# Optimization experiments

Hardware: AMD Instinct MI355X
Metric: run time of the kernel (lower is better)

## Reference

```python
import jax, jax.numpy as jnp
import numpy as np

N, IN, OUT = 262144, 256, 256
EPS_MIN = 1e-10


def setup_inputs() -> dict:
    key = jax.random.key(0)
    k1, k2, k3 = jax.random.split(key, 3)
    x = jax.random.normal(k1, (N, IN), dtype=jnp.float32)
    weight = jax.random.normal(k2, (OUT, IN), dtype=jnp.float32) * 0.05
    bias = jax.random.normal(k3, (OUT,), dtype=jnp.float32) * 0.02
    return {"x": x, "weight": weight, "bias": bias}


def reference(x, weight, bias):
    # Mean-center weight rows and input rows (dim=1 in torch)
    wc = weight - jnp.mean(weight, axis=1, keepdims=True)          # [out, in]
    xc = x - jnp.mean(x, axis=1, keepdims=True)                    # [N, in]
    # temp_linear with all-ones weight == row-sum of xc^2, broadcast over out
    x_len = jax.lax.stop_gradient(
        jnp.sqrt(jnp.sum(xc * xc, axis=1, keepdims=True)))          # [N, 1]
    # temp_linear(ones_like(x)) with weight wc^2 == row-sum of wc^2 per out
    w_len = jax.lax.stop_gradient(
        jnp.sqrt(jnp.sum(wc * wc, axis=1)))                          # [out]
    # Correlation: centered GEMM, normalized, clamped; bias added after clamp
    corr = jnp.einsum('ni,oi->no', xc, wc) / (x_len * w_len[None, :])
    out = jnp.clip(corr, EPS_MIN, None) + bias[None, :]
    return out
```

## Files before the change

kernel.cpp:

```cpp
#include <hip/hip_runtime.h>
#include <hip/hip_bf16.h>


#define K_DIM 256
#define N_OUT 256
#define BM 64
#define LDS_STRIDE 264

typedef __attribute__((ext_vector_type(8))) __bf16 bf16x8;
typedef __attribute__((ext_vector_type(8))) unsigned short u16x8;
typedef __attribute__((ext_vector_type(4))) float f32x4;

__device__ __forceinline__ unsigned short f2bf(float f) {
    union { float f; unsigned u; } v; v.f = f;
    unsigned r = v.u + 0x7FFFu + ((v.u >> 16) & 1u);
    return (unsigned short)(r >> 16);
}

__global__ __launch_bounds__(64) void prep_w(const float* __restrict__ w,
                                             unsigned short* __restrict__ wcb) {
    int o = blockIdx.x;
    int lane = threadIdx.x;
    f32x4 v = *((const f32x4*)(w + (size_t)o * K_DIM) + lane);
    float s  = v.x + v.y + v.z + v.w;
    float s2 = v.x*v.x + v.y*v.y + v.z*v.z + v.w*v.w;
#pragma unroll
    for (int off = 32; off >= 1; off >>= 1) {
        s  += __shfl_xor(s,  off);
        s2 += __shfl_xor(s2, off);
    }
    float mean  = s * (1.0f / 256.0f);
    float var   = s2 - s * mean;
    float scale = rsqrtf(fmaxf(var, 1e-30f));
    ushort4 b;
    b.x = f2bf((v.x - mean) * scale);
    b.y = f2bf((v.y - mean) * scale);
    b.z = f2bf((v.z - mean) * scale);
    b.w = f2bf((v.w - mean) * scale);
    *(ushort4*)(wcb + (size_t)o * K_DIM + lane * 4) = b;
}

__global__ __launch_bounds__(256, 4) void pcc_gemm(const float* __restrict__ x,
                                                   const unsigned short* __restrict__ wcb,
                                                   const float* __restrict__ bias,
                                                   float* __restrict__ out) {
    __shared__ unsigned short xs[BM * LDS_STRIDE];
    __shared__ float nrm[BM];

    const int t    = threadIdx.x;
    const int wave = t >> 6;
    const int lane = t & 63;
    const int l15  = lane & 15;
    const int q    = lane >> 4;
    const size_t row0 = (size_t)blockIdx.x * BM;

    const int srow = wave * 16 + l15;
    const float* rp = x + (row0 + srow) * K_DIM + q * 64;

    f32x4 v[16];
#pragma unroll
    for (int j = 0; j < 16; ++j) v[j] = ((const f32x4*)rp)[j];

    const int n0 = wave * 64;
    float bv[4];
#pragma unroll
    for (int ni = 0; ni < 4; ++ni) bv[ni] = bias[n0 + ni * 16 + l15];

    unsigned short* wp = xs + srow * LDS_STRIDE + q * 64;
#pragma unroll
    for (int j = 0; j < 8; ++j) {
        u16x8 p;
        p[0] = f2bf(v[2*j].x);   p[1] = f2bf(v[2*j].y);
        p[2] = f2bf(v[2*j].z);   p[3] = f2bf(v[2*j].w);
        p[4] = f2bf(v[2*j+1].x); p[5] = f2bf(v[2*j+1].y);
        p[6] = f2bf(v[2*j+1].z); p[7] = f2bf(v[2*j+1].w);
        *(u16x8*)(wp + j * 8) = p;
    }

    float s = 0.f, s2 = 0.f;
#pragma unroll
    for (int j = 0; j < 16; ++j) {
        s += v[j].x + v[j].y + v[j].z + v[j].w;
        s2 = fmaf(v[j].x, v[j].x, s2);
        s2 = fmaf(v[j].y, v[j].y, s2);
        s2 = fmaf(v[j].z, v[j].z, s2);
        s2 = fmaf(v[j].w, v[j].w, s2);
    }
    s  += __shfl_xor(s, 16);  s  += __shfl_xor(s, 32);
    s2 += __shfl_xor(s2, 16); s2 += __shfl_xor(s2, 32);
    float var = s2 - s * s * (1.0f / 256.0f);
    float inv = rsqrtf(fmaxf(var, 1e-30f));
    if (q == 0) nrm[srow] = inv;
    __syncthreads();

    f32x4 acc[4][4];
#pragma unroll
    for (int mi = 0; mi < 4; ++mi)
#pragma unroll
        for (int ni = 0; ni < 4; ++ni)
            acc[mi][ni] = (f32x4){0.f, 0.f, 0.f, 0.f};

    const unsigned short* wbase = wcb + (size_t)n0 * K_DIM + q * 8;

#pragma unroll
    for (int ks = 0; ks < 8; ++ks) {
        bf16x8 a[4], b[4];
#pragma unroll
        for (int mi = 0; mi < 4; ++mi)
            a[mi] = *(const bf16x8*)(xs + (mi * 16 + l15) * LDS_STRIDE + ks * 32 + q * 8);
#pragma unroll
        for (int ni = 0; ni < 4; ++ni)
            b[ni] = *(const bf16x8*)(wbase + (size_t)(ni * 16 + l15) * K_DIM + ks * 32);
#pragma unroll
        for (int mi = 0; mi < 4; ++mi)
#pragma unroll
            for (int ni = 0; ni < 4; ++ni)
                acc[mi][ni] = __builtin_amdgcn_mfma_f32_16x16x32_bf16(a[mi], b[ni], acc[mi][ni], 0, 0, 0);
    }

    float invv[4][4];
#pragma unroll
    for (int mi = 0; mi < 4; ++mi)
#pragma unroll
        for (int r = 0; r < 4; ++r)
            invv[mi][r] = nrm[mi * 16 + q * 4 + r];

    float* obase = out + row0 * N_OUT;
#pragma unroll
    for (int mi = 0; mi < 4; ++mi) {
#pragma unroll
        for (int r = 0; r < 4; ++r) {
            const int orow = mi * 16 + q * 4 + r;
            float* op = obase + (size_t)orow * N_OUT + n0 + l15;
#pragma unroll
            for (int ni = 0; ni < 4; ++ni)
                op[ni * 16] = fmaxf(acc[mi][ni][r] * invv[mi][r], 1e-10f) + bv[ni];
        }
    }
}

extern "C" void kernel_launch(void* const* d_in, const int* in_sizes, int n_in,
                              void* d_out, int out_size, void* d_ws, size_t ws_size,
                              hipStream_t stream) {
    const float* x    = (const float*)d_in[0];
    const float* w    = (const float*)d_in[1];
    const float* bias = (const float*)d_in[2];
    float* out = (float*)d_out;
    unsigned short* wcb = (unsigned short*)d_ws;

    prep_w<<<256, 64, 0, stream>>>(w, wcb);
    pcc_gemm<<<262144 / BM, 256, 0, stream>>>(x, wcb, bias, out);
}
```

Measured before the change: 474.5 us.

## Stage full weight matrix in LDS and stream x rows per wave

The GEMM kernel becomes persistent-style, launching 512 blocks of 512 threads. Each block loads the whole bf16 centered weight matrix and the bias into LDS once, and each wave then processes 4 chunks of 16 rows. X rows go straight from global memory into MFMA A-fragments, so the per-tile LDS staging of x and the global reads of weight fragments are gone. Output is written as f32x4 non-temporal stores. In exchange, a block needs about 135KB of LDS and each wave holds 64 accumulator registers, which limits occupancy and the overlap of x loads with compute.

```diff
diff --git a/kernel.cpp b/kernel.cpp
--- a/kernel.cpp
+++ b/kernel.cpp
@@ -2,14 +2,15 @@
 #include <hip/hip_bf16.h>
 
 
-#define K_DIM 256
-#define N_OUT 256
-#define BM 64
-#define LDS_STRIDE 264
+#define K_DIM  256
+#define N_OUT  256
+#define LDSW   264
+#define CHUNKS 4
+#define NBLK   512
 
 typedef __attribute__((ext_vector_type(8))) __bf16 bf16x8;
 typedef __attribute__((ext_vector_type(8))) unsigned short u16x8;
-typedef __attribute__((ext_vector_type(4))) float f32x4;
+typedef __attribute__((ext_vector_type(4))) float  f32x4;
 
 __device__ __forceinline__ unsigned short f2bf(float f) {
     union { float f; unsigned u; } v; v.f = f;
@@ -40,101 +41,83 @@
     *(ushort4*)(wcb + (size_t)o * K_DIM + lane * 4) = b;
 }
 
-__global__ __launch_bounds__(256, 4) void pcc_gemm(const float* __restrict__ x,
+__global__ __launch_bounds__(512, 2) void pcc_gemm(const float* __restrict__ x,
                                                    const unsigned short* __restrict__ wcb,
                                                    const float* __restrict__ bias,
                                                    float* __restrict__ out) {
-    __shared__ unsigned short xs[BM * LDS_STRIDE];
-    __shared__ float nrm[BM];
+    __shared__ __align__(16) unsigned short bs[256 * LDSW];
+    __shared__ __align__(16) float bias_s[N_OUT];
 
     const int t    = threadIdx.x;
-    const int wave = t >> 6;
+    const int w    = t >> 6;
     const int lane = t & 63;
     const int l15  = lane & 15;
     const int q    = lane >> 4;
-    const size_t row0 = (size_t)blockIdx.x * BM;
 
-    const int srow = wave * 16 + l15;
-    const float* rp = x + (row0 + srow) * K_DIM + q * 64;
-
-    f32x4 v[16];
+    {
+        const int r = t >> 1, h = t & 1;
+        const unsigned short* src = wcb + (size_t)r * K_DIM + h * 128;
+        unsigned short* dst = bs + r * LDSW + h * 128;
 #pragma unroll
-    for (int j = 0; j < 16; ++j) v[j] = ((const f32x4*)rp)[j];
-
-    const int n0 = wave * 64;
-    float bv[4];
-#pragma unroll
-    for (int ni = 0; ni < 4; ++ni) bv[ni] = bias[n0 + ni * 16 + l15];
-
-    unsigned short* wp = xs + srow * LDS_STRIDE + q * 64;
-#pragma unroll
-    for (int j = 0; j < 8; ++j) {
-        u16x8 p;
-        p[0] = f2bf(v[2*j].x);   p[1] = f2bf(v[2*j].y);
-        p[2] = f2bf(v[2*j].z);   p[3] = f2bf(v[2*j].w);
-        p[4] = f2bf(v[2*j+1].x); p[5] = f2bf(v[2*j+1].y);
-        p[6] = f2bf(v[2*j+1].z); p[7] = f2bf(v[2*j+1].w);
-        *(u16x8*)(wp + j * 8) = p;
+        for (int j = 0; j < 16; ++j)
+            *(u16x8*)(dst + j * 8) = *(const u16x8*)(src + j * 8);
+        if (t < 64) *(f32x4*)(bias_s + t * 4) = *(const f32x4*)(bias + t * 4);
     }
-
-    float s = 0.f, s2 = 0.f;
-#pragma unroll
-    for (int j = 0; j < 16; ++j) {
-        s += v[j].x + v[j].y + v[j].z + v[j].w;
-        s2 = fmaf(v[j].x, v[j].x, s2);
-        s2 = fmaf(v[j].y, v[j].y, s2);
-        s2 = fmaf(v[j].z, v[j].z, s2);
-        s2 = fmaf(v[j].w, v[j].w, s2);
-    }
-    s  += __shfl_xor(s, 16);  s  += __shfl_xor(s, 32);
-    s2 += __shfl_xor(s2, 16); s2 += __shfl_xor(s2, 32);
-    float var = s2 - s * s * (1.0f / 256.0f);
-    float inv = rsqrtf(fmaxf(var, 1e-30f));
-    if (q == 0) nrm[srow] = inv;
     __syncthreads();
 
-    f32x4 acc[4][4];
+    const size_t wrow0 = ((size_t)blockIdx.x * 8 + w) * (16 * CHUNKS);
+
+#pragma unroll 1
+    for (int c = 0; c < CHUNKS; ++c) {
+        const size_t row = wrow0 + c * 16 + l15;
+        const float* rp = x + row * K_DIM + q * 8;
+
+        bf16x8 af[8];
+        float s = 0.f, s2 = 0.f;
 #pragma unroll
-    for (int mi = 0; mi < 4; ++mi)
+        for (int ks = 0; ks < 8; ++ks) {
+            f32x4 lo = *(const f32x4*)(rp + ks * 32);
+            f32x4 hi = *(const f32x4*)(rp + ks * 32 + 4);
+            s += lo.x + lo.y + lo.z + lo.w;
+            s += hi.x + hi.y + hi.z + hi.w;
+            s2 = fmaf(lo.x, lo.x, s2); s2 = fmaf(lo.y, lo.y, s2);
+            s2 = fmaf(lo.z, lo.z, s2); s2 = fmaf(lo.w, lo.w, s2);
+            s2 = fmaf(hi.x, hi.x, s2); s2 = fmaf(hi.y, hi.y, s2);
+            s2 = fmaf(hi.z, hi.z, s2); s2 = fmaf(hi.w, hi.w, s2);
+            bf16x8 a;
+            a[0] = (__bf16)lo.x; a[1] = (__bf16)lo.y;
+            a[2] = (__bf16)lo.z; a[3] = (__bf16)lo.w;
+            a[4] = (__bf16)hi.x; a[5] = (__bf16)hi.y;
+            a[6] = (__bf16)hi.z; a[7] = (__bf16)hi.w;
+            af[ks] = a;
+        }
+        s  += __shfl_xor(s, 16);  s  += __shfl_xor(s, 32);
+        s2 += __shfl_xor(s2, 16); s2 += __shfl_xor(s2, 32);
+        const float inv = rsqrtf(fmaxf(s2 - s * s * (1.0f / 256.0f), 1e-30f));
+
+        f32x4 acc[16];
 #pragma unroll
-        for (int ni = 0; ni < 4; ++ni)
-            acc[mi][ni] = (f32x4){0.f, 0.f, 0.f, 0.f};
+        for (int ni = 0; ni < 16; ++ni) acc[ni] = (f32x4){0.f, 0.f, 0.f, 0.f};
 
-    const unsigned short* wbase = wcb + (size_t)n0 * K_DIM + q * 8;
+        const unsigned short* bbase = bs + l15 * LDSW + q * 8;
+#pragma unroll
+        for (int ks = 0; ks < 8; ++ks) {
+#pragma unroll
+            for (int ni = 0; ni < 16; ++ni) {
+                bf16x8 b = *(const bf16x8*)(bbase + ni * 16 * LDSW + ks * 32);
+                acc[ni] = __builtin_amdgcn_mfma_f32_16x16x32_bf16(b, af[ks], acc[ni], 0, 0, 0);
+            }
+        }
 
+        float* op = out + row * N_OUT + q * 4;
 #pragma unroll
-    for (int ks = 0; ks < 8; ++ks) {
-        bf16x8 a[4], b[4];
+        for (int ni = 0; ni < 16; ++ni) {
+            f32x4 bv = *(const f32x4*)(bias_s + ni * 16 + q * 4);
+            f32x4 vx;
 #pragma unroll
-        for (int mi = 0; mi < 4; ++mi)
-            a[mi] = *(const bf16x8*)(xs + (mi * 16 + l15) * LDS_STRIDE + ks * 32 + q * 8);
-#pragma unroll
-        for (int ni = 0; ni < 4; ++ni)
-            b[ni] = *(const bf16x8*)(wbase + (size_t)(ni * 16 + l15) * K_DIM + ks * 32);
-#pragma unroll
-        for (int mi = 0; mi < 4; ++mi)
-#pragma unroll
-            for (int ni = 0; ni < 4; ++ni)
-                acc[mi][ni] = __builtin_amdgcn_mfma_f32_16x16x32_bf16(a[mi], b[ni], acc[mi][ni], 0, 0, 0);
-    }
-
-    float invv[4][4];
-#pragma unroll
-    for (int mi = 0; mi < 4; ++mi)
-#pragma unroll
-        for (int r = 0; r < 4; ++r)
-            invv[mi][r] = nrm[mi * 16 + q * 4 + r];
-
-    float* obase = out + row0 * N_OUT;
-#pragma unroll
-    for (int mi = 0; mi < 4; ++mi) {
-#pragma unroll
-        for (int r = 0; r < 4; ++r) {
-            const int orow = mi * 16 + q * 4 + r;
-            float* op = obase + (size_t)orow * N_OUT + n0 + l15;
-#pragma unroll
-            for (int ni = 0; ni < 4; ++ni)
-                op[ni * 16] = fmaxf(acc[mi][ni][r] * invv[mi][r], 1e-10f) + bv[ni];
+            for (int r = 0; r < 4; ++r)
+                vx[r] = fmaxf(acc[ni][r] * inv, 1e-10f) + bv[r];
+            __builtin_nontemporal_store(vx, (f32x4*)(op + ni * 16));
         }
     }
 }
@@ -149,5 +132,5 @@
     unsigned short* wcb = (unsigned short*)d_ws;
 
     prep_w<<<256, 64, 0, stream>>>(w, wcb);
-    pcc_gemm<<<262144 / BM, 256, 0, stream>>>(x, wcb, bias, out);
+    pcc_gemm<<<NBLK, 512, 0, stream>>>(x, wcb, bias, out);
 }
```

After: 876.9 us. +84.8%, slower.
